# Optimization experiments

Measured on AMD Instinct MI355X. Metric: run time of the kernel, lower is better.

The kernel has to match this reference:

```python
import jax, jax.numpy as jnp
import numpy as np

N_HEAD = 8
NEG = -1e9


def setup_inputs() -> dict:
    key = jax.random.key(0)
    ks = jax.random.split(key, 12)
    B, S, D = 16, 512, 512
    query = jax.random.normal(ks[0], (B, S, D), dtype=jnp.float32)
    inputs = jax.random.normal(ks[1], (B, S, D), dtype=jnp.float32)
    # repetition-count matrix (nonnegative ints, used via log10(x+1))
    ren_mat = jax.random.randint(ks[2], (B, S, S), 0, 10).astype(jnp.float32)
    # signed time-gap matrix (used via exp(-|t|))
    timestamp = jax.random.normal(ks[3], (B, S, S), dtype=jnp.float32) * 3.0
    # causal future mask: True above the diagonal (k=1)
    mask = jnp.triu(jnp.ones((1, S, S), dtype=bool), k=1)
    scale = 0.02
    Wq = jax.random.normal(ks[4], (D, D), dtype=jnp.float32) * scale
    Wk = jax.random.normal(ks[5], (D, D), dtype=jnp.float32) * scale
    Wv = jax.random.normal(ks[6], (D, D), dtype=jnp.float32) * scale
    Wo = jax.random.normal(ks[7], (D, D), dtype=jnp.float32) * scale
    W1 = jax.random.normal(ks[8], (D, D), dtype=jnp.float32) * scale
    bq = jnp.zeros((D,), jnp.float32); bk = jnp.zeros((D,), jnp.float32)
    bv = jnp.zeros((D,), jnp.float32); bo = jnp.zeros((D,), jnp.float32)
    b1 = jnp.zeros((D,), jnp.float32)
    ln_g = jnp.ones((D,), jnp.float32); ln_b = jnp.zeros((D,), jnp.float32)
    l1 = jax.random.uniform(ks[9], (1,), dtype=jnp.float32)  # nn.Parameter(torch.rand(1))
    gammas = jax.random.normal(ks[10], (N_HEAD, 1, 1), dtype=jnp.float32) * 0.1
    return {"query": query, "inputs": inputs, "ren_mat": ren_mat,
            "timestamp": timestamp, "mask": mask,
            "Wq": Wq, "bq": bq, "Wk": Wk, "bk": bk, "Wv": Wv, "bv": bv,
            "Wo": Wo, "bo": bo, "W1": W1, "b1": b1,
            "ln_g": ln_g, "ln_b": ln_b, "l1": l1, "gammas": gammas}


def reference(query, inputs, ren_mat, timestamp, mask,
              Wq, bq, Wk, bk, Wv, bv, Wo, bo, W1, b1, ln_g, ln_b, l1, gammas):
    B, S, D = inputs.shape
    H = N_HEAD
    hd = D // H

    def proj(x, W, b):
        # nn.Linear: x @ W.T + b, then split heads -> (B, H, S, hd)
        return (x @ W.T + b).reshape(B, S, H, hd).transpose(0, 2, 1, 3)

    q = proj(inputs, Wq, bq)
    k = proj(inputs, Wk, bk)
    v = proj(inputs, Wv, bv)

    m = mask[:, None]  # (1,1,S,S)
    # softplus(gammas) is computed in the original but unused by the math
    _ = jax.nn.softplus(gammas)

    scores = jnp.einsum('bhqd,bhkd->bhqk', q, k) / np.float32(np.sqrt(hd))
    prob_attn = jax.nn.softmax(jnp.where(m, NEG, scores), axis=-1)

    # memory-decay branch: log10 recency + exp time-decay, softmax-fused
    ren_feat = jnp.where(m, NEG, jnp.log10(ren_mat[:, None] + 1.0))   # (B,1,S,S)
    time_feat = jnp.where(m, NEG, jnp.exp(-jnp.abs(timestamp[:, None])))
    mem_attn = jax.nn.softmax(ren_feat + time_feat, axis=-1)          # (B,1,S,S)

    l = l1[0]
    p = (1.0 - l) * prob_attn + l * mem_attn  # broadcast over heads (== repeat)

    out = jnp.einsum('bhqk,bhkd->bhqd', p, v)
    out = out.transpose(0, 2, 1, 3).reshape(B, S, D)
    out = out @ Wo.T + bo            # MHA lin_out
    out = out + (out @ W1.T + b1)    # SMFE residual (dropout off in eval)
    # LayerNorm (biased variance, eps=1e-5)
    mu = out.mean(-1, keepdims=True)
    var = jnp.mean((out - mu) ** 2, axis=-1, keepdims=True)
    out = (out - mu) / jnp.sqrt(var + 1e-5) * ln_g + ln_b
    return out
```

## Files before the change

kernel.cpp:

```cpp
#include <hip/hip_runtime.h>
#include <hip/hip_bf16.h>

constexpr int B = 16, S = 512, D = 512, H = 8, HD = 64;
constexpr int BS = B * S;

typedef __attribute__((ext_vector_type(8))) short bf16x8;
typedef __attribute__((ext_vector_type(4))) float f32x4;

#define DEVI __device__ __forceinline__

DEVI bf16x8 ldbf8(const __hip_bfloat16* p) {
    return *reinterpret_cast<const bf16x8*>(p);
}

DEVI unsigned short bfbits(float f) {
    __hip_bfloat16 h = __float2bfloat16(f);
    return __builtin_bit_cast(unsigned short, h);
}

DEVI void gload_lds16(const void* g, void* l) {
    __builtin_amdgcn_global_load_lds((const __attribute__((address_space(1))) void*)g,
                                     (__attribute__((address_space(3))) void*)l, 16, 0, 0);
}

__global__ __launch_bounds__(256) void cvt_kernel(const float* __restrict__ src,
                                                  __hip_bfloat16* __restrict__ dst,
                                                  int n4) {
    int i = blockIdx.x * 256 + threadIdx.x;
    if (i >= n4) return;
    float4 v = reinterpret_cast<const float4*>(src)[i];
    unsigned int lo = (unsigned int)bfbits(v.x) | ((unsigned int)bfbits(v.y) << 16);
    unsigned int hi = (unsigned int)bfbits(v.z) | ((unsigned int)bfbits(v.w) << 16);
    uint2 o; o.x = lo; o.y = hi;
    reinterpret_cast<uint2*>(dst)[i] = o;
}

__global__ __launch_bounds__(256) void wcvt_kernel(const float* __restrict__ s0,
                                                   const float* __restrict__ s1,
                                                   const float* __restrict__ s2,
                                                   const float* __restrict__ s3,
                                                   const float* __restrict__ s4,
                                                   __hip_bfloat16* __restrict__ dst) {
    int idx = blockIdx.x * 256 + threadIdx.x;
    int wsel = idx >> 16;
    int off = idx & 65535;
    const float* s;
    switch (wsel) {
        case 0: s = s0; break;
        case 1: s = s1; break;
        case 2: s = s2; break;
        case 3: s = s3; break;
        default: s = s4; break;
    }
    float4 v = reinterpret_cast<const float4*>(s)[off];
    unsigned int lo = (unsigned int)bfbits(v.x) | ((unsigned int)bfbits(v.y) << 16);
    unsigned int hi = (unsigned int)bfbits(v.z) | ((unsigned int)bfbits(v.w) << 16);
    uint2 o; o.x = lo; o.y = hi;
    reinterpret_cast<uint2*>(dst)[idx] = o;
}

__global__ __launch_bounds__(256) void mem_attn_kernel(const float* __restrict__ ren,
                                                       const float* __restrict__ ts,
                                                       __hip_bfloat16* __restrict__ mem) {
    int tid = threadIdx.x;
    int w = tid >> 6, l = tid & 63;
    int row = blockIdx.x * 4 + w;
    int qr = row & (S - 1);
    size_t base = (size_t)row * S + l * 8;
    float f[8];
    bool active = (l * 8 <= qr);
    if (active) {
        float4 r0 = *reinterpret_cast<const float4*>(ren + base);
        float4 r1 = *reinterpret_cast<const float4*>(ren + base + 4);
        float4 t0 = *reinterpret_cast<const float4*>(ts + base);
        float4 t1 = *reinterpret_cast<const float4*>(ts + base + 4);
        float rv[8] = {r0.x, r0.y, r0.z, r0.w, r1.x, r1.y, r1.z, r1.w};
        float tv[8] = {t0.x, t0.y, t0.z, t0.w, t1.x, t1.y, t1.z, t1.w};
#pragma unroll
        for (int j = 0; j < 8; ++j) {
            int c = l * 8 + j;
            f[j] = (c <= qr) ? (__log2f(rv[j] + 1.0f) * 0.3010299957f + __expf(-fabsf(tv[j])))
                             : -3.0e38f;
        }
    } else {
#pragma unroll
        for (int j = 0; j < 8; ++j) f[j] = -3.0e38f;
    }
    float m = -3.0e38f;
#pragma unroll
    for (int j = 0; j < 8; ++j) m = fmaxf(m, f[j]);
#pragma unroll
    for (int off = 32; off >= 1; off >>= 1) m = fmaxf(m, __shfl_xor(m, off));
    float s = 0.f;
#pragma unroll
    for (int j = 0; j < 8; ++j) { float e = __expf(f[j] - m); f[j] = e; s += e; }
#pragma unroll
    for (int off = 32; off >= 1; off >>= 1) s += __shfl_xor(s, off);
    float inv = 1.0f / s;
    bf16x8 o;
#pragma unroll
    for (int j = 0; j < 8; ++j) o[j] = (short)bfbits(f[j] * inv);
    *reinterpret_cast<bf16x8*>(mem + base) = o;
}


DEVI void stage_tiles(const __hip_bfloat16* __restrict__ A,
                      const __hip_bfloat16* __restrict__ W,
                      int rowBase, int colBase, int kt, short* ldsbuf, int tid) {
#pragma unroll
    for (int c = 0; c < 2; ++c) {
        int o = c * 256 + tid;
        int row = o & 127, ch = o >> 7;
        gload_lds16(A + (size_t)(rowBase + row) * 512 + kt * 32 + ch * 8,
                    (char*)ldsbuf + o * 16);
        gload_lds16(W + (size_t)(colBase + row) * 512 + kt * 32 + ch * 8,
                    (char*)ldsbuf + 8192 + o * 16);
    }
}

DEVI void gemm_mainloop(const __hip_bfloat16* __restrict__ A,
                        const __hip_bfloat16* __restrict__ W,
                        int rowBase, int colBase, int ktiles,
                        short* lds, f32x4 (&acc)[4][4]) {
    int tid = threadIdx.x;
    int w = tid >> 6, l = tid & 63, lr = l & 15, lg = l >> 4;
    int wR = w >> 1, wC = w & 1;
    stage_tiles(A, W, rowBase, colBase, 0, lds, tid);
    __syncthreads();
    for (int t = 0; t < ktiles; ++t) {
        if (t + 1 < ktiles)
            stage_tiles(A, W, rowBase, colBase, t + 1, lds + ((t + 1) & 1) * 8192, tid);
        const short* ab = lds + (t & 1) * 8192;
        const short* bb = ab + 4096;
        bf16x8 af[4], bfr[4];
#pragma unroll
        for (int m = 0; m < 4; ++m)
            af[m] = *reinterpret_cast<const bf16x8*>(ab + (lg * 128 + wR * 64 + m * 16 + lr) * 8);
#pragma unroll
        for (int n = 0; n < 4; ++n)
            bfr[n] = *reinterpret_cast<const bf16x8*>(bb + (lg * 128 + wC * 64 + n * 16 + lr) * 8);
#pragma unroll
        for (int m = 0; m < 4; ++m)
#pragma unroll
            for (int n = 0; n < 4; ++n)
                acc[m][n] = __builtin_amdgcn_mfma_f32_16x16x32_bf16(af[m], bfr[n], acc[m][n], 0, 0, 0);
        __syncthreads();
    }
}

__global__ __launch_bounds__(256) void gemm_qkv_s(const __hip_bfloat16* __restrict__ A,
                                                  const __hip_bfloat16* __restrict__ Wqkv,
                                                  const float* __restrict__ bq,
                                                  const float* __restrict__ bk,
                                                  const float* __restrict__ bv,
                                                  __hip_bfloat16* __restrict__ q_out,
                                                  __hip_bfloat16* __restrict__ k_out,
                                                  __hip_bfloat16* __restrict__ vT_out) {
    __shared__ short lds[16384];
    int tid = threadIdx.x;
    int w = tid >> 6, l = tid & 63, lr = l & 15, lg = l >> 4;
    int wR = w >> 1, wC = w & 1;
    int mat = blockIdx.y >> 2;
    int rowBase = blockIdx.x * 128;
    int colBase = (blockIdx.y & 3) * 128;
    const float* bias = (mat == 0) ? bq : (mat == 1) ? bk : bv;
    const __hip_bfloat16* W = Wqkv + (size_t)mat * 262144;

    f32x4 acc[4][4];
#pragma unroll
    for (int m = 0; m < 4; ++m)
#pragma unroll
        for (int n = 0; n < 4; ++n) acc[m][n] = (f32x4){0.f, 0.f, 0.f, 0.f};

    gemm_mainloop(A, W, rowBase, colBase, 16, lds, acc);
    short* ep = lds + w * 4096;
    float bsv[4];
#pragma unroll
    for (int n = 0; n < 4; ++n) bsv[n] = bias[colBase + wC * 64 + n * 16 + lr];

    if (mat < 2) {
        __hip_bfloat16* o = (mat == 0) ? q_out : k_out;
#pragma unroll
        for (int m = 0; m < 4; ++m)
#pragma unroll
            for (int n = 0; n < 4; ++n)
#pragma unroll
                for (int i = 0; i < 4; ++i) {
                    int rr = m * 16 + lg * 4 + i, cl = n * 16 + lr;
                    ep[rr * 64 + (cl ^ ((rr & 7) << 3))] = (short)bfbits(acc[m][n][i] + bsv[n]);
                }
        int h_ = (colBase + wC * 64) >> 6;
#pragma unroll
        for (int p = 0; p < 8; ++p) {
            int rr = p * 8 + (l >> 3), ch = l & 7;
            bf16x8 v = *reinterpret_cast<const bf16x8*>(ep + rr * 64 + ((ch ^ (rr & 7)) << 3));
            int grow = rowBase + wR * 64 + rr;
            int b_ = grow >> 9, s_ = grow & 511;
            *reinterpret_cast<bf16x8*>(o + (((size_t)(b_ * 8 + h_) * 512 + s_) << 6) + ch * 8) = v;
        }
    } else {
#pragma unroll
        for (int m = 0; m < 4; ++m)
#pragma unroll
            for (int n = 0; n < 4; ++n)
#pragma unroll
                for (int i = 0; i < 4; ++i) {
                    int ss = m * 16 + lg * 4 + i, dd = n * 16 + lr;
                    ep[dd * 64 + (ss ^ ((dd & 7) << 3))] = (short)bfbits(acc[m][n][i] + bsv[n]);
                }
        int h_ = (colBase + wC * 64) >> 6;
        int s0g = rowBase + wR * 64;
        int b_ = s0g >> 9, sb = s0g & 511;
#pragma unroll
        for (int p = 0; p < 8; ++p) {
            int dd = p * 8 + (l >> 3), ch = l & 7;
            bf16x8 v = *reinterpret_cast<const bf16x8*>(ep + dd * 64 + ((ch ^ (dd & 7)) << 3));
            *reinterpret_cast<bf16x8*>(vT_out + (((size_t)(b_ * 8 + h_) * 64 + dd) << 9) + sb + ch * 8) = v;
        }
    }
}

template <int MODE>
__global__ __launch_bounds__(256) void gemm_bt_s(const __hip_bfloat16* __restrict__ A,
                                                 const __hip_bfloat16* __restrict__ W,
                                                 const float* __restrict__ bias,
                                                 float* __restrict__ outf,
                                                 __hip_bfloat16* __restrict__ outb,
                                                 const float* __restrict__ resid) {
    __shared__ short lds[16384];
    int tid = threadIdx.x;
    int w = tid >> 6, l = tid & 63, lr = l & 15, lg = l >> 4;
    int wR = w >> 1, wC = w & 1;
    int rowBase = blockIdx.x * 128;
    int colBase = blockIdx.y * 128;

    f32x4 acc[4][4];
#pragma unroll
    for (int m = 0; m < 4; ++m)
#pragma unroll
        for (int n = 0; n < 4; ++n) acc[m][n] = (f32x4){0.f, 0.f, 0.f, 0.f};

    gemm_mainloop(A, W, rowBase, colBase, 16, lds, acc);

#pragma unroll
    for (int n = 0; n < 4; ++n) {
        int col = colBase + wC * 64 + n * 16 + lr;
        float bs = bias[col];
#pragma unroll
        for (int m = 0; m < 4; ++m) {
#pragma unroll
            for (int i = 0; i < 4; ++i) {
                int row = rowBase + wR * 64 + m * 16 + lg * 4 + i;
                float val = acc[m][n][i] + bs;
                size_t idx = (size_t)row * 512 + col;
                if constexpr (MODE == 2) {
                    outf[idx] = val;
                    outb[idx] = __float2bfloat16(val);
                } else {
                    outf[idx] = val + resid[idx];
                }
            }
        }
    }
}

__global__ __launch_bounds__(256) void gemm_memv_s(const __hip_bfloat16* __restrict__ A,
                                                   const __hip_bfloat16* __restrict__ VT,
                                                   __hip_bfloat16* __restrict__ outb) {
    __shared__ short lds[16384];
    int tid = threadIdx.x;
    int w = tid >> 6, l = tid & 63, lr = l & 15, lg = l >> 4;
    int wR = w >> 1, wC = w & 1;
    int rowBase = blockIdx.x * 128;
    int colBase = blockIdx.y * 128;
    int b_ = rowBase >> 9;
    const __hip_bfloat16* W = VT + (size_t)b_ * 262144;
    int ktiles = ((blockIdx.x & 3) + 1) * 4;

    f32x4 acc[4][4];
#pragma unroll
    for (int m = 0; m < 4; ++m)
#pragma unroll
        for (int n = 0; n < 4; ++n) acc[m][n] = (f32x4){0.f, 0.f, 0.f, 0.f};

    gemm_mainloop(A, W, rowBase, colBase, ktiles, lds, acc);

    short* ep = lds + w * 4096;
#pragma unroll
    for (int m = 0; m < 4; ++m)
#pragma unroll
        for (int n = 0; n < 4; ++n)
#pragma unroll
            for (int i = 0; i < 4; ++i) {
                int rr = m * 16 + lg * 4 + i, cl = n * 16 + lr;
                ep[rr * 64 + (cl ^ ((rr & 7) << 3))] = (short)bfbits(acc[m][n][i]);
            }
#pragma unroll
    for (int p = 0; p < 8; ++p) {
        int rr = p * 8 + (l >> 3), ch = l & 7;
        bf16x8 v = *reinterpret_cast<const bf16x8*>(ep + rr * 64 + ((ch ^ (rr & 7)) << 3));
        int grow = rowBase + wR * 64 + rr;
        *reinterpret_cast<bf16x8*>(outb + (size_t)grow * 512 + colBase + wC * 64 + ch * 8) = v;
    }
}

__global__ __launch_bounds__(256, 3) void attn2_kernel(const __hip_bfloat16* __restrict__ Q,
                                                       const __hip_bfloat16* __restrict__ Km,
                                                       const __hip_bfloat16* __restrict__ VT,
                                                       const __hip_bfloat16* __restrict__ memv,
                                                       const float* __restrict__ l1,
                                                       __hip_bfloat16* __restrict__ outb) {
    __shared__ short lds[20480];
    short* Kb = lds;
    short* Vb = lds + 8192;
    int tid = threadIdx.x;
    int w = tid >> 6, l = tid & 63;
    int lr = l & 15, lg = l >> 4;
    int blk = blockIdx.x;
    int bh = blk & 127, qt = blk >> 7;
    int b = bh >> 3, h = bh & 7;
    int q0 = qt * 64;
    int nt = qt + 1;
    short* Pw = lds + 16384 + w * 1024;

    const char* Kg = (const char*)Km + (size_t)bh * 65536;
    const char* Vg = (const char*)VT + (size_t)bh * 65536;

    int o0 = w * 64 + l;
    const __hip_bfloat16* qp = Q + ((size_t)bh * 512 + q0 + w * 16 + lr) * 64 + lg * 8;
    bf16x8 qa0 = ldbf8(qp), qa1 = ldbf8(qp + 32);
    float lam = l1[0];

#pragma unroll
    for (int c = 0; c < 2; ++c) {
        int o = c * 256 + o0;
        int r = o >> 3, c16 = o & 7;
        int sw = ((c16 ^ (r & 7)) << 4);
        gload_lds16(Kg + r * 128 + sw, (char*)Kb + o * 16);
        gload_lds16(Vg + r * 1024 + sw, (char*)Vb + o * 16);
    }
    __syncthreads();

    f32x4 acc2[4];
#pragma unroll
    for (int n = 0; n < 4; ++n) acc2[n] = (f32x4){0.f, 0.f, 0.f, 0.f};
    float mrun[4] = {-3e38f, -3e38f, -3e38f, -3e38f};
    float psum[4] = {0.f, 0.f, 0.f, 0.f};

    for (int t = 0; t < nt; ++t) {
        if (t + 1 < nt) {
#pragma unroll
            for (int c = 0; c < 2; ++c) {
                int o = c * 256 + o0;
                int r = o >> 3, c16 = o & 7;
                int sw = ((c16 ^ (r & 7)) << 4);
                gload_lds16(Kg + (t + 1) * 8192 + r * 128 + sw,
                            (char*)Kb + ((t + 1) & 1) * 8192 + o * 16);
                gload_lds16(Vg + r * 1024 + (t + 1) * 128 + sw,
                            (char*)Vb + ((t + 1) & 1) * 8192 + o * 16);
            }
        }
        const short* kb = Kb + (t & 1) * 4096;
        const short* vb = Vb + (t & 1) * 4096;

        f32x4 s4[4];
#pragma unroll
        for (int j = 0; j < 4; ++j) {
            int row = j * 16 + lr;
            int sw = row & 7;
            bf16x8 k0 = *reinterpret_cast<const bf16x8*>(kb + row * 64 + ((lg ^ sw) << 3));
            bf16x8 k1 = *reinterpret_cast<const bf16x8*>(kb + row * 64 + (((4 + lg) ^ sw) << 3));
            f32x4 cc = {0.f, 0.f, 0.f, 0.f};
            cc = __builtin_amdgcn_mfma_f32_16x16x32_bf16(qa0, k0, cc, 0, 0, 0);
            cc = __builtin_amdgcn_mfma_f32_16x16x32_bf16(qa1, k1, cc, 0, 0, 0);
            s4[j] = cc;
        }

        if (t == nt - 1) {
#pragma unroll
            for (int j = 0; j < 4; ++j) {
                int col = t * 64 + j * 16 + lr;
#pragma unroll
                for (int i = 0; i < 4; ++i) {
                    int rowg = q0 + w * 16 + lg * 4 + i;
                    s4[j][i] = (col <= rowg) ? s4[j][i] * 0.125f : -3e38f;
                }
            }
        } else {
#pragma unroll
            for (int j = 0; j < 4; ++j)
#pragma unroll
                for (int i = 0; i < 4; ++i) s4[j][i] *= 0.125f;
        }

        float tmax[4];
#pragma unroll
        for (int i = 0; i < 4; ++i)
            tmax[i] = fmaxf(fmaxf(s4[0][i], s4[1][i]), fmaxf(s4[2][i], s4[3][i]));
#pragma unroll
        for (int off = 1; off < 16; off <<= 1)
#pragma unroll
            for (int i = 0; i < 4; ++i) tmax[i] = fmaxf(tmax[i], __shfl_xor(tmax[i], off));

        float e[4][4];
#pragma unroll
        for (int i = 0; i < 4; ++i) {
            float mnew = fmaxf(mrun[i], tmax[i]);
            float sc = __expf(mrun[i] - mnew);
            mrun[i] = mnew;
            float ps = 0.f;
#pragma unroll
            for (int j = 0; j < 4; ++j) {
                float ee = __expf(s4[j][i] - mnew);
                e[j][i] = ee;
                ps += ee;
            }
            psum[i] = psum[i] * sc + ps;
#pragma unroll
            for (int n = 0; n < 4; ++n) acc2[n][i] *= sc;
        }

#pragma unroll
        for (int j = 0; j < 4; ++j)
#pragma unroll
            for (int i = 0; i < 4; ++i) {
                int rr = lg * 4 + i;
                int cc = j * 16 + lr;
                Pw[rr * 64 + (cc ^ ((rr & 7) << 3))] = (short)bfbits(e[j][i]);
            }

#pragma unroll
        for (int ksub = 0; ksub < 2; ++ksub) {
            bf16x8 pa = *reinterpret_cast<const bf16x8*>(
                Pw + lr * 64 + (((ksub * 4 + lg) ^ (lr & 7)) << 3));
#pragma unroll
            for (int n = 0; n < 4; ++n) {
                int d = n * 16 + lr;
                bf16x8 vf = *reinterpret_cast<const bf16x8*>(
                    vb + d * 64 + (((ksub * 4 + lg) ^ (d & 7)) << 3));
                acc2[n] = __builtin_amdgcn_mfma_f32_16x16x32_bf16(pa, vf, acc2[n], 0, 0, 0);
            }
        }
        __syncthreads();
    }

#pragma unroll
    for (int off = 1; off < 16; off <<= 1)
#pragma unroll
        for (int i = 0; i < 4; ++i) psum[i] += __shfl_xor(psum[i], off);
    float rinv[4];
#pragma unroll
    for (int i = 0; i < 4; ++i) rinv[i] = (1.0f - lam) / psum[i];

    const __hip_bfloat16* mvp = memv + ((size_t)b * 512 + q0 + w * 16 + lg * 4) * 512 + h * 64;
    __hip_bfloat16* op = outb + ((size_t)b * 512 + q0 + w * 16 + lg * 4) * 512 + h * 64;
#pragma unroll
    for (int n = 0; n < 4; ++n)
#pragma unroll
        for (int i = 0; i < 4; ++i) {
            float mv = __bfloat162float(mvp[(size_t)i * 512 + n * 16 + lr]);
            op[(size_t)i * 512 + n * 16 + lr] =
                __float2bfloat16(acc2[n][i] * rinv[i] + lam * mv);
        }
}

__global__ __launch_bounds__(256) void ln_kernel(float* __restrict__ io,
                                                 const float* __restrict__ g,
                                                 const float* __restrict__ bb) {
    int tid = threadIdx.x;
    int w = tid >> 6, l = tid & 63;
    size_t row = (size_t)blockIdx.x * 4 + w;
    float* p = io + row * 512 + l * 8;
    float4 x0 = *reinterpret_cast<float4*>(p);
    float4 x1 = *reinterpret_cast<float4*>(p + 4);
    float xs[8] = {x0.x, x0.y, x0.z, x0.w, x1.x, x1.y, x1.z, x1.w};
    float s = 0.f;
#pragma unroll
    for (int j = 0; j < 8; ++j) s += xs[j];
#pragma unroll
    for (int off = 32; off >= 1; off >>= 1) s += __shfl_xor(s, off);
    float mu = s * (1.0f / 512.0f);
    float vs = 0.f;
#pragma unroll
    for (int j = 0; j < 8; ++j) { float d = xs[j] - mu; vs += d * d; }
#pragma unroll
    for (int off = 32; off >= 1; off >>= 1) vs += __shfl_xor(vs, off);
    float rstd = rsqrtf(vs * (1.0f / 512.0f) + 1e-5f);
    const float4 g0 = *reinterpret_cast<const float4*>(g + l * 8);
    const float4 g1 = *reinterpret_cast<const float4*>(g + l * 8 + 4);
    const float4 b0 = *reinterpret_cast<const float4*>(bb + l * 8);
    const float4 b1 = *reinterpret_cast<const float4*>(bb + l * 8 + 4);
    float gs[8] = {g0.x, g0.y, g0.z, g0.w, g1.x, g1.y, g1.z, g1.w};
    float bs[8] = {b0.x, b0.y, b0.z, b0.w, b1.x, b1.y, b1.z, b1.w};
    float ys[8];
#pragma unroll
    for (int j = 0; j < 8; ++j) ys[j] = (xs[j] - mu) * rstd * gs[j] + bs[j];
    float4 y0 = make_float4(ys[0], ys[1], ys[2], ys[3]);
    float4 y1 = make_float4(ys[4], ys[5], ys[6], ys[7]);
    *reinterpret_cast<float4*>(p) = y0;
    *reinterpret_cast<float4*>(p + 4) = y1;
}

extern "C" void kernel_launch(void* const* d_in, const int* in_sizes, int n_in,
                              void* d_out, int out_size, void* d_ws, size_t ws_size,
                              hipStream_t stream) {
    const float* inputs = (const float*)d_in[1];
    const float* ren    = (const float*)d_in[2];
    const float* ts     = (const float*)d_in[3];
    const float* Wq = (const float*)d_in[5];
    const float* bq = (const float*)d_in[6];
    const float* Wk = (const float*)d_in[7];
    const float* bk = (const float*)d_in[8];
    const float* Wv = (const float*)d_in[9];
    const float* bv = (const float*)d_in[10];
    const float* Wo = (const float*)d_in[11];
    const float* bo = (const float*)d_in[12];
    const float* W1 = (const float*)d_in[13];
    const float* b1 = (const float*)d_in[14];
    const float* ln_g = (const float*)d_in[15];
    const float* ln_b = (const float*)d_in[16];
    const float* l1   = (const float*)d_in[17];
    float* out = (float*)d_out;

    char* ws = (char*)d_ws;
    __hip_bfloat16* in_bf = (__hip_bfloat16*)(ws + 0);
    __hip_bfloat16* ao_bf = (__hip_bfloat16*)(ws + 0);
    __hip_bfloat16* wq_bf = (__hip_bfloat16*)(ws + 8388608);
    __hip_bfloat16* wo_bf = (__hip_bfloat16*)(ws + 9961472);
    __hip_bfloat16* w1_bf = (__hip_bfloat16*)(ws + 10485760);
    __hip_bfloat16* q_bf  = (__hip_bfloat16*)(ws + 11010048);
    __hip_bfloat16* o1_bf = (__hip_bfloat16*)(ws + 11010048);
    __hip_bfloat16* k_bf  = (__hip_bfloat16*)(ws + 19398656);
    __hip_bfloat16* vT_bf = (__hip_bfloat16*)(ws + 27787264);
    __hip_bfloat16* mem_bf = (__hip_bfloat16*)(ws + 36175872);
    float*          out1_f = (float*)(ws + 36175872);
    __hip_bfloat16* memv_bf = (__hip_bfloat16*)(ws + 69730304);

    cvt_kernel<<<4096, 256, 0, stream>>>(inputs, in_bf, BS * D / 4);
    wcvt_kernel<<<1280, 256, 0, stream>>>(Wq, Wk, Wv, Wo, W1, wq_bf);

    gemm_qkv_s<<<dim3(64, 12), 256, 0, stream>>>(in_bf, wq_bf, bq, bk, bv, q_bf, k_bf, vT_bf);

    mem_attn_kernel<<<BS / 4, 256, 0, stream>>>(ren, ts, mem_bf);

    gemm_memv_s<<<dim3(64, 4), 256, 0, stream>>>(mem_bf, vT_bf, memv_bf);

    attn2_kernel<<<1024, 256, 0, stream>>>(q_bf, k_bf, vT_bf, memv_bf, l1, ao_bf);

    gemm_bt_s<2><<<dim3(64, 4), 256, 0, stream>>>(ao_bf, wo_bf, bo, out1_f, o1_bf, nullptr);

    gemm_bt_s<3><<<dim3(64, 4), 256, 0, stream>>>(o1_bf, w1_bf, b1, out, nullptr, out1_f);

    ln_kernel<<<BS / 4, 256, 0, stream>>>(out, ln_g, ln_b);
}
```

Before: 257.3 us.

## Fold Wo and W1 into one effective weight and fuse mem·V into attention

```diff
diff --git a/kernel.cpp b/kernel.cpp
--- a/kernel.cpp
+++ b/kernel.cpp
@@ -35,12 +35,11 @@
     reinterpret_cast<uint2*>(dst)[i] = o;
 }
 
-__global__ __launch_bounds__(256) void wcvt_kernel(const float* __restrict__ s0,
-                                                   const float* __restrict__ s1,
-                                                   const float* __restrict__ s2,
-                                                   const float* __restrict__ s3,
-                                                   const float* __restrict__ s4,
-                                                   __hip_bfloat16* __restrict__ dst) {
+__global__ __launch_bounds__(256) void wcvt4_kernel(const float* __restrict__ s0,
+                                                    const float* __restrict__ s1,
+                                                    const float* __restrict__ s2,
+                                                    const float* __restrict__ s3,
+                                                    __hip_bfloat16* __restrict__ dst) {
     int idx = blockIdx.x * 256 + threadIdx.x;
     int wsel = idx >> 16;
     int off = idx & 65535;
@@ -49,14 +48,46 @@
         case 0: s = s0; break;
         case 1: s = s1; break;
         case 2: s = s2; break;
-        case 3: s = s3; break;
-        default: s = s4; break;
+        default: s = s3; break;
     }
     float4 v = reinterpret_cast<const float4*>(s)[off];
     unsigned int lo = (unsigned int)bfbits(v.x) | ((unsigned int)bfbits(v.y) << 16);
     unsigned int hi = (unsigned int)bfbits(v.z) | ((unsigned int)bfbits(v.w) << 16);
     uint2 o; o.x = lo; o.y = hi;
     reinterpret_cast<uint2*>(dst)[idx] = o;
+}
+
+__global__ __launch_bounds__(256) void wtr_kernel(const float* __restrict__ Wo,
+                                                  __hip_bfloat16* __restrict__ WoT) {
+    __shared__ float t64[64][65];
+    int bx = blockIdx.x & 7, by = blockIdx.x >> 3;
+    int tc = threadIdx.x & 63, tr = threadIdx.x >> 6;
+#pragma unroll
+    for (int i = 0; i < 16; ++i) {
+        int row = tr * 16 + i;
+        t64[row][tc] = Wo[(size_t)(by * 64 + row) * 512 + bx * 64 + tc];
+    }
+    __syncthreads();
+#pragma unroll
+    for (int i = 0; i < 16; ++i) {
+        int row = tr * 16 + i;
+        WoT[(size_t)(bx * 64 + row) * 512 + by * 64 + tc] = __float2bfloat16(t64[tc][row]);
+    }
+}
+
+__global__ __launch_bounds__(256) void bprep_kernel(const float* __restrict__ W1,
+                                                    const float* __restrict__ bo,
+                                                    const float* __restrict__ b1,
+                                                    float* __restrict__ beff) {
+    int j = blockIdx.x * 256 + threadIdx.x;
+    float s = 0.f;
+    const float4* wr = reinterpret_cast<const float4*>(W1 + (size_t)j * 512);
+    const float4* br = reinterpret_cast<const float4*>(bo);
+    for (int m = 0; m < 128; ++m) {
+        float4 a = wr[m], b = br[m];
+        s += a.x * b.x + a.y * b.y + a.z * b.z + a.w * b.w;
+    }
+    beff[j] = bo[j] + s + b1[j];
 }
 
 __global__ __launch_bounds__(256) void mem_attn_kernel(const float* __restrict__ ren,
@@ -103,7 +134,6 @@
     *reinterpret_cast<bf16x8*>(mem + base) = o;
 }
 
-
 DEVI void stage_tiles(const __hip_bfloat16* __restrict__ A,
                       const __hip_bfloat16* __restrict__ W,
                       int rowBase, int colBase, int kt, short* ldsbuf, int tid) {
@@ -220,13 +250,10 @@
     }
 }
 
-template <int MODE>
-__global__ __launch_bounds__(256) void gemm_bt_s(const __hip_bfloat16* __restrict__ A,
-                                                 const __hip_bfloat16* __restrict__ W,
-                                                 const float* __restrict__ bias,
-                                                 float* __restrict__ outf,
-                                                 __hip_bfloat16* __restrict__ outb,
-                                                 const float* __restrict__ resid) {
+__global__ __launch_bounds__(256) void gemm_weff(const __hip_bfloat16* __restrict__ W1b,
+                                                 const __hip_bfloat16* __restrict__ WoT,
+                                                 const float* __restrict__ Wof,
+                                                 __hip_bfloat16* __restrict__ weff) {
     __shared__ short lds[16384];
     int tid = threadIdx.x;
     int w = tid >> 6, l = tid & 63, lr = l & 15, lg = l >> 4;
@@ -240,42 +267,32 @@
 #pragma unroll
         for (int n = 0; n < 4; ++n) acc[m][n] = (f32x4){0.f, 0.f, 0.f, 0.f};
 
-    gemm_mainloop(A, W, rowBase, colBase, 16, lds, acc);
+    gemm_mainloop(W1b, WoT, rowBase, colBase, 16, lds, acc);
 
 #pragma unroll
     for (int n = 0; n < 4; ++n) {
         int col = colBase + wC * 64 + n * 16 + lr;
-        float bs = bias[col];
-#pragma unroll
-        for (int m = 0; m < 4; ++m) {
+#pragma unroll
+        for (int m = 0; m < 4; ++m)
 #pragma unroll
             for (int i = 0; i < 4; ++i) {
                 int row = rowBase + wR * 64 + m * 16 + lg * 4 + i;
-                float val = acc[m][n][i] + bs;
                 size_t idx = (size_t)row * 512 + col;
-                if constexpr (MODE == 2) {
-                    outf[idx] = val;
-                    outb[idx] = __float2bfloat16(val);
-                } else {
-                    outf[idx] = val + resid[idx];
-                }
-            }
-        }
-    }
-}
-
-__global__ __launch_bounds__(256) void gemm_memv_s(const __hip_bfloat16* __restrict__ A,
-                                                   const __hip_bfloat16* __restrict__ VT,
-                                                   __hip_bfloat16* __restrict__ outb) {
+                weff[idx] = __float2bfloat16(acc[m][n][i] + Wof[idx]);
+            }
+    }
+}
+
+__global__ __launch_bounds__(256) void gemm_final(const __hip_bfloat16* __restrict__ A,
+                                                  const __hip_bfloat16* __restrict__ W,
+                                                  const float* __restrict__ bias,
+                                                  float* __restrict__ outf) {
     __shared__ short lds[16384];
     int tid = threadIdx.x;
     int w = tid >> 6, l = tid & 63, lr = l & 15, lg = l >> 4;
     int wR = w >> 1, wC = w & 1;
     int rowBase = blockIdx.x * 128;
     int colBase = blockIdx.y * 128;
-    int b_ = rowBase >> 9;
-    const __hip_bfloat16* W = VT + (size_t)b_ * 262144;
-    int ktiles = ((blockIdx.x & 3) + 1) * 4;
 
     f32x4 acc[4][4];
 #pragma unroll
@@ -283,31 +300,26 @@
 #pragma unroll
         for (int n = 0; n < 4; ++n) acc[m][n] = (f32x4){0.f, 0.f, 0.f, 0.f};
 
-    gemm_mainloop(A, W, rowBase, colBase, ktiles, lds, acc);
-
-    short* ep = lds + w * 4096;
-#pragma unroll
-    for (int m = 0; m < 4; ++m)
-#pragma unroll
-        for (int n = 0; n < 4; ++n)
+    gemm_mainloop(A, W, rowBase, colBase, 16, lds, acc);
+
+#pragma unroll
+    for (int n = 0; n < 4; ++n) {
+        int col = colBase + wC * 64 + n * 16 + lr;
+        float bs = bias[col];
+#pragma unroll
+        for (int m = 0; m < 4; ++m)
 #pragma unroll
             for (int i = 0; i < 4; ++i) {
-                int rr = m * 16 + lg * 4 + i, cl = n * 16 + lr;
-                ep[rr * 64 + (cl ^ ((rr & 7) << 3))] = (short)bfbits(acc[m][n][i]);
-            }
-#pragma unroll
-    for (int p = 0; p < 8; ++p) {
-        int rr = p * 8 + (l >> 3), ch = l & 7;
-        bf16x8 v = *reinterpret_cast<const bf16x8*>(ep + rr * 64 + ((ch ^ (rr & 7)) << 3));
-        int grow = rowBase + wR * 64 + rr;
-        *reinterpret_cast<bf16x8*>(outb + (size_t)grow * 512 + colBase + wC * 64 + ch * 8) = v;
-    }
-}
-
-__global__ __launch_bounds__(256, 3) void attn2_kernel(const __hip_bfloat16* __restrict__ Q,
+                int row = rowBase + wR * 64 + m * 16 + lg * 4 + i;
+                outf[(size_t)row * 512 + col] = acc[m][n][i] + bs;
+            }
+    }
+}
+
+__global__ __launch_bounds__(256, 2) void attn3_kernel(const __hip_bfloat16* __restrict__ Q,
                                                        const __hip_bfloat16* __restrict__ Km,
                                                        const __hip_bfloat16* __restrict__ VT,
-                                                       const __hip_bfloat16* __restrict__ memv,
+                                                       const __hip_bfloat16* __restrict__ mem,
                                                        const float* __restrict__ l1,
                                                        __hip_bfloat16* __restrict__ outb) {
     __shared__ short lds[20480];
@@ -329,6 +341,7 @@
     int o0 = w * 64 + l;
     const __hip_bfloat16* qp = Q + ((size_t)bh * 512 + q0 + w * 16 + lr) * 64 + lg * 8;
     bf16x8 qa0 = ldbf8(qp), qa1 = ldbf8(qp + 32);
+    const __hip_bfloat16* memrow = mem + ((size_t)b * 512 + q0 + w * 16 + lr) * 512;
     float lam = l1[0];
 
 #pragma unroll
@@ -341,9 +354,12 @@
     }
     __syncthreads();
 
-    f32x4 acc2[4];
-#pragma unroll
-    for (int n = 0; n < 4; ++n) acc2[n] = (f32x4){0.f, 0.f, 0.f, 0.f};
+    f32x4 acc2[4], acc3[4];
+#pragma unroll
+    for (int n = 0; n < 4; ++n) {
+        acc2[n] = (f32x4){0.f, 0.f, 0.f, 0.f};
+        acc3[n] = (f32x4){0.f, 0.f, 0.f, 0.f};
+    }
     float mrun[4] = {-3e38f, -3e38f, -3e38f, -3e38f};
     float psum[4] = {0.f, 0.f, 0.f, 0.f};
 
@@ -360,6 +376,8 @@
                             (char*)Vb + ((t + 1) & 1) * 8192 + o * 16);
             }
         }
+        bf16x8 ma0 = ldbf8(memrow + t * 64 + lg * 8);
+        bf16x8 ma1 = ldbf8(memrow + t * 64 + 32 + lg * 8);
         const short* kb = Kb + (t & 1) * 4096;
         const short* vb = Vb + (t & 1) * 4096;
 
@@ -433,12 +451,14 @@
         for (int ksub = 0; ksub < 2; ++ksub) {
             bf16x8 pa = *reinterpret_cast<const bf16x8*>(
                 Pw + lr * 64 + (((ksub * 4 + lg) ^ (lr & 7)) << 3));
+            bf16x8 mfrag = (ksub == 0) ? ma0 : ma1;
 #pragma unroll
             for (int n = 0; n < 4; ++n) {
                 int d = n * 16 + lr;
                 bf16x8 vf = *reinterpret_cast<const bf16x8*>(
                     vb + d * 64 + (((ksub * 4 + lg) ^ (d & 7)) << 3));
                 acc2[n] = __builtin_amdgcn_mfma_f32_16x16x32_bf16(pa, vf, acc2[n], 0, 0, 0);
+                acc3[n] = __builtin_amdgcn_mfma_f32_16x16x32_bf16(mfrag, vf, acc3[n], 0, 0, 0);
             }
         }
         __syncthreads();
@@ -452,16 +472,13 @@
 #pragma unroll
     for (int i = 0; i < 4; ++i) rinv[i] = (1.0f - lam) / psum[i];
 
-    const __hip_bfloat16* mvp = memv + ((size_t)b * 512 + q0 + w * 16 + lg * 4) * 512 + h * 64;
     __hip_bfloat16* op = outb + ((size_t)b * 512 + q0 + w * 16 + lg * 4) * 512 + h * 64;
 #pragma unroll
     for (int n = 0; n < 4; ++n)
 #pragma unroll
-        for (int i = 0; i < 4; ++i) {
-            float mv = __bfloat162float(mvp[(size_t)i * 512 + n * 16 + lr]);
+        for (int i = 0; i < 4; ++i)
             op[(size_t)i * 512 + n * 16 + lr] =
-                __float2bfloat16(acc2[n][i] * rinv[i] + lam * mv);
-        }
+                __float2bfloat16(acc2[n][i] * rinv[i] + lam * acc3[n][i]);
 }
 
 __global__ __launch_bounds__(256) void ln_kernel(float* __restrict__ io,
@@ -523,33 +540,31 @@
     float* out = (float*)d_out;
 
     char* ws = (char*)d_ws;
-    __hip_bfloat16* in_bf = (__hip_bfloat16*)(ws + 0);
-    __hip_bfloat16* ao_bf = (__hip_bfloat16*)(ws + 0);
-    __hip_bfloat16* wq_bf = (__hip_bfloat16*)(ws + 8388608);
-    __hip_bfloat16* wo_bf = (__hip_bfloat16*)(ws + 9961472);
-    __hip_bfloat16* w1_bf = (__hip_bfloat16*)(ws + 10485760);
-    __hip_bfloat16* q_bf  = (__hip_bfloat16*)(ws + 11010048);
-    __hip_bfloat16* o1_bf = (__hip_bfloat16*)(ws + 11010048);
-    __hip_bfloat16* k_bf  = (__hip_bfloat16*)(ws + 19398656);
-    __hip_bfloat16* vT_bf = (__hip_bfloat16*)(ws + 27787264);
-    __hip_bfloat16* mem_bf = (__hip_bfloat16*)(ws + 36175872);
-    float*          out1_f = (float*)(ws + 36175872);
-    __hip_bfloat16* memv_bf = (__hip_bfloat16*)(ws + 69730304);
+    __hip_bfloat16* in_bf  = (__hip_bfloat16*)(ws + 0);
+    __hip_bfloat16* ao_bf  = (__hip_bfloat16*)(ws + 0);
+    __hip_bfloat16* wq_bf  = (__hip_bfloat16*)(ws + 8388608);
+    __hip_bfloat16* w1_bf  = (__hip_bfloat16*)(ws + 8388608 + 3 * 524288);
+    __hip_bfloat16* woT_bf = (__hip_bfloat16*)(ws + 10485760);
+    __hip_bfloat16* weff_bf= (__hip_bfloat16*)(ws + 11010048);
+    float*          beff_f = (float*)(ws + 11534336);
+    __hip_bfloat16* q_bf   = (__hip_bfloat16*)(ws + 11538432);
+    __hip_bfloat16* k_bf   = (__hip_bfloat16*)(ws + 19927040);
+    __hip_bfloat16* vT_bf  = (__hip_bfloat16*)(ws + 28315648);
+    __hip_bfloat16* mem_bf = (__hip_bfloat16*)(ws + 36704256);
 
     cvt_kernel<<<4096, 256, 0, stream>>>(inputs, in_bf, BS * D / 4);
-    wcvt_kernel<<<1280, 256, 0, stream>>>(Wq, Wk, Wv, Wo, W1, wq_bf);
+    wcvt4_kernel<<<1024, 256, 0, stream>>>(Wq, Wk, Wv, W1, wq_bf);
+    wtr_kernel<<<64, 256, 0, stream>>>(Wo, woT_bf);
+    bprep_kernel<<<2, 256, 0, stream>>>(W1, bo, b1, beff_f);
+    gemm_weff<<<dim3(4, 4), 256, 0, stream>>>(w1_bf, woT_bf, Wo, weff_bf);
 
     gemm_qkv_s<<<dim3(64, 12), 256, 0, stream>>>(in_bf, wq_bf, bq, bk, bv, q_bf, k_bf, vT_bf);
 
     mem_attn_kernel<<<BS / 4, 256, 0, stream>>>(ren, ts, mem_bf);
 
-    gemm_memv_s<<<dim3(64, 4), 256, 0, stream>>>(mem_bf, vT_bf, memv_bf);
-
-    attn2_kernel<<<1024, 256, 0, stream>>>(q_bf, k_bf, vT_bf, memv_bf, l1, ao_bf);
-
-    gemm_bt_s<2><<<dim3(64, 4), 256, 0, stream>>>(ao_bf, wo_bf, bo, out1_f, o1_bf, nullptr);
-
-    gemm_bt_s<3><<<dim3(64, 4), 256, 0, stream>>>(o1_bf, w1_bf, b1, out, nullptr, out1_f);
+    attn3_kernel<<<1024, 256, 0, stream>>>(q_bf, k_bf, vT_bf, mem_bf, l1, ao_bf);
+
+    gemm_final<<<dim3(64, 4), 256, 0, stream>>>(ao_bf, weff_bf, beff_f, out);
 
     ln_kernel<<<BS / 4, 256, 0, stream>>>(out, ln_g, ln_b);
 }
```

New measurement: 253.8 us. About the same (-1.4%).
